# Kernel optimization log

Hardware: AMD Instinct MI355X
Metric: run time of the kernel (lower is better)

The kernel has to match this reference:

```python
import jax, jax.numpy as jnp
import numpy as np

E = 512        # emb_size
H = 2 * E      # LSTM units
B = 512        # beam/query batch (batched Python-loop states)
K = 32         # padded candidates per state
T = 8          # max_path_length
N_ENT = 50000
N_REL = 5000


def setup_inputs() -> dict:
    key = jax.random.key(0)
    ks = jax.random.split(key, 12)
    f32 = jnp.float32
    ent_emb = jax.random.normal(ks[0], (N_ENT, E), f32) * 0.05
    rel_emb = jax.random.normal(ks[1], (N_REL, E), f32) * 0.05
    relation = jax.random.normal(ks[2], (B, E), f32) * 0.05
    Wx = jax.random.normal(ks[3], (H, 4 * H), f32) * 0.02
    Wh = jax.random.normal(ks[4], (H, 4 * H), f32) * 0.02
    b = jnp.zeros((4 * H,), f32)
    W1 = jax.random.normal(ks[5], (4 * E, 3 * E), f32) * 0.02
    b1 = jnp.zeros((3 * E,), f32)
    W2 = jax.random.normal(ks[6], (3 * E, 2 * E), f32) * 0.02
    b2 = jnp.zeros((2 * E,), f32)
    current_ids = jax.random.randint(ks[7], (T, B), 0, N_ENT)
    prev_rel_ids = jax.random.randint(ks[8], (T, B), 0, N_REL)
    cand_rel_ids = jax.random.randint(ks[9], (T, B, K), 0, N_REL)
    cand_ent_ids = jax.random.randint(ks[10], (T, B, K), 0, N_ENT)
    return {
        "ent_emb": ent_emb, "rel_emb": rel_emb, "relation": relation,
        "Wx": Wx, "Wh": Wh, "b": b,
        "W1": W1, "b1": b1, "W2": W2, "b2": b2,
        "current_ids": current_ids, "prev_rel_ids": prev_rel_ids,
        "cand_rel_ids": cand_rel_ids, "cand_ent_ids": cand_ent_ids,
    }


def reference(ent_emb, rel_emb, relation, Wx, Wh, b, W1, b1, W2, b2,
              current_ids, prev_rel_ids, cand_rel_ids, cand_ent_ids):
    Bh = relation.shape[0]
    units = Wh.shape[0]
    h0 = jnp.zeros((Bh, units), ent_emb.dtype)
    c0 = jnp.zeros((Bh, units), ent_emb.dtype)

    def step(carry, xs):
        h, c = carry
        cur, prl, crel, cent = xs
        # LSTMCell input: concat(prev relation vec, current entity vec)  [B, 2E]
        x = jnp.concatenate([rel_emb[prl], ent_emb[cur]], axis=-1)
        z = x @ Wx + h @ Wh + b                      # [B, 4H], keras gate order i,f,g,o
        i_, f_, g_, o_ = jnp.split(z, 4, axis=-1)
        c = jax.nn.sigmoid(f_) * c + jax.nn.sigmoid(i_) * jnp.tanh(g_)
        h = jax.nn.sigmoid(o_) * jnp.tanh(c)
        # posterior MLP on concat(ent, history, relation)  [B, 4E] -> [B, 2E]
        feat = jax.nn.relu(jnp.concatenate([ent_emb[cur], h, relation], axis=-1) @ W1 + b1)
        feat = jax.nn.relu(feat @ W2 + b2)
        # candidate embeddings: concat(rel vec, to-entity vec)  [B, K, 2E]
        cand = jnp.concatenate([rel_emb[crel], ent_emb[cent]], axis=-1)
        probs = jax.nn.softmax(jnp.einsum('bkd,bd->bk', cand, feat), axis=-1)
        return (h, c), probs

    _, probs = jax.lax.scan(step, (h0, c0),
                            (current_ids, prev_rel_ids, cand_rel_ids, cand_ent_ids))
    return probs  # [T, B, K]
```

## Files before the change

kernel.cpp:

```cpp
#include <hip/hip_runtime.h>
#include <stdint.h>

typedef __attribute__((ext_vector_type(4))) float f32x4;
typedef __attribute__((ext_vector_type(8))) __bf16 bf16x8;
typedef __attribute__((ext_vector_type(8))) unsigned short u16x8;
typedef __attribute__((ext_vector_type(4))) unsigned short u16x4;

typedef const __attribute__((address_space(1))) unsigned int gu32;
typedef __attribute__((address_space(3))) unsigned int lu32;

__device__ __forceinline__ float b2f(unsigned short u) {
  unsigned int x = ((unsigned int)u) << 16;
  float f; __builtin_memcpy(&f, &x, 4); return f;
}
__device__ __forceinline__ unsigned short f2b(float f) {
  unsigned int x; __builtin_memcpy(&x, &f, 4);
  x += 0x7fffu + ((x >> 16) & 1u);
  return (unsigned short)(x >> 16);
}
__device__ __forceinline__ float sigmoidf(float x) {
  return 1.f / (1.f + __expf(-x));
}
__device__ __forceinline__ float tanh_fast(float x) {
  return 1.f - 2.f / (1.f + __expf(2.f * x));
}

__global__ __launch_bounds__(256) void prep1(
    const float* __restrict__ Wx, unsigned short* __restrict__ WxT,
    const float* __restrict__ Wh, unsigned short* __restrict__ WhT,
    const float* __restrict__ W1, unsigned short* __restrict__ W1T,
    const float* __restrict__ W2, unsigned short* __restrict__ W2T,
    const float* __restrict__ ent, const float* __restrict__ rel,
    const float* __restrict__ rln,
    const int* __restrict__ cur, const int* __restrict__ prl,
    unsigned short* __restrict__ Xall, unsigned short* __restrict__ ERall) {
  __shared__ unsigned short tile[64][72];
  const int tid = threadIdx.x;
  int b = blockIdx.x;
  if (b < 3200) {
    const float* in; unsigned short* out; int R, C, bx, by;
    if (b < 1024)      { in = Wx; out = WxT; R = 1024; C = 4096; bx = b & 63; by = b >> 6; }
    else if (b < 2048) { b -= 1024; in = Wh; out = WhT; R = 1024; C = 4096; bx = b & 63; by = b >> 6; }
    else if (b < 2816) { b -= 2048; in = W1; out = W1T; R = 2048; C = 1536; bx = b % 24; by = b / 24; }
    else               { b -= 2816; in = W2; out = W2T; R = 1536; C = 1024; bx = b & 15; by = b >> 4; }
    const int r0 = by * 64, c0 = bx * 64;
    const int r = tid >> 3;
    const int c8 = (tid & 7) * 8;
#pragma unroll
    for (int i = 0; i < 2; i++) {
      const int rr = r + 32*i;
      const float* src = in + (size_t)(r0 + rr) * C + c0 + c8;
      f32x4 a = *(const f32x4*)src;
      f32x4 bb = *(const f32x4*)(src + 4);
      unsigned short tmp[8];
#pragma unroll
      for (int j = 0; j < 4; j++) { tmp[j] = f2b(a[j]); tmp[4+j] = f2b(bb[j]); }
      *(u16x8*)(&tile[rr][c8 ^ (((rr >> 3) & 7) << 3)]) = *(u16x8*)tmp;
    }
    __syncthreads();
    const int rswz = (tid & 7) << 3;
#pragma unroll
    for (int i = 0; i < 2; i++) {
      const int ro = r + 32*i;
      unsigned short tmp[8];
#pragma unroll
      for (int j = 0; j < 8; j++) tmp[j] = tile[c8 + j][ro ^ rswz];
      *(u16x8*)(out + (size_t)(c0 + ro) * R + r0 + c8) = *(u16x8*)tmp;
    }
  } else {
    const int row = b - 3200;
    const int bb = row & 511;
    const int ci = cur[row], ri = prl[row];
    const int half = tid >> 7;
    const int j = tid & 127;
    const float* src;
    if (half == 0) src = (j < 64) ? (rel + (size_t)ri * 512 + j * 8)
                                  : (ent + (size_t)ci * 512 + (j - 64) * 8);
    else           src = (j < 64) ? (ent + (size_t)ci * 512 + j * 8)
                                  : (rln + (size_t)bb * 512 + (j - 64) * 8);
    f32x4 a = *(const f32x4*)src, c = *(const f32x4*)(src + 4);
    unsigned short t[8];
#pragma unroll
    for (int q = 0; q < 4; q++) { t[q] = f2b(a[q]); t[4+q] = f2b(c[q]); }
    unsigned short* dst = (half == 0 ? Xall : ERall) + (size_t)row * 1024 + j * 8;
    *(u16x8*)dst = *(u16x8*)t;
  }
}

template<bool HAS_BIAS, bool DO_RELU, bool PERM_B, bool ASPLIT, bool LSTM0, bool FUSE_CONV>
__global__ __launch_bounds__(256) void gemm_bf16(
    const unsigned short* __restrict__ A,
    const unsigned short* __restrict__ A2, int lda,
    const unsigned short* __restrict__ BT, int ldb, int K,
    const float* __restrict__ bias,
    unsigned short* __restrict__ Cout, int ldc,
    const float* __restrict__ gbias,
    unsigned short* __restrict__ Hout, float* __restrict__ Cst,
    const float* __restrict__ entF, unsigned short* __restrict__ entB,
    const float* __restrict__ relF, unsigned short* __restrict__ relB) {
  __shared__ unsigned short As[128][64];
  __shared__ unsigned short Bs[128][64];
  const int tid = threadIdx.x;
  if (FUSE_CONV && blockIdx.y >= 32) {
    const long long N0 = 50000LL * 512 / 8, N1 = 5000LL * 512 / 8;
    long long i = ((long long)(blockIdx.y - 32) * gridDim.x + blockIdx.x) * 256 + tid;
    if (i >= N0 + N1) return;
    const float* in; unsigned short* out;
    if (i < N0) { in = entF; out = entB; }
    else        { in = relF; out = relB; i -= N0; }
    f32x4 a = *(const f32x4*)(in + i * 8);
    f32x4 c = *(const f32x4*)(in + i * 8 + 4);
    unsigned short t[8];
#pragma unroll
    for (int q = 0; q < 4; q++) { t[q] = f2b(a[q]); t[4+q] = f2b(c[q]); }
    *(u16x8*)(out + i * 8) = *(u16x8*)t;
    return;
  }
  const int lane = tid & 63;
  const int w = tid >> 6;
  const int wr = w >> 1, wc = w & 1;
  const int m0 = blockIdx.y * 128, n0 = blockIdx.x * 128;
  f32x4 acc[4][4] = {};
  const int srow = lane >> 3;
  const int scol = ((lane & 7) ^ srow) * 8;

  for (int k0 = 0; k0 < K; k0 += 64) {
    const unsigned short* asrc; int ac;
    if (ASPLIT) {
      if (k0 < 512)       { asrc = A;  ac = k0; }
      else if (k0 < 1536) { asrc = A2; ac = k0 - 512; }
      else                { asrc = A;  ac = k0 - 1024; }
    } else { asrc = A; ac = k0; }
#pragma unroll
    for (int i = 0; i < 4; i++) {
      const int c = w * 4 + i;
      const int row = c * 8 + srow;
      __builtin_amdgcn_global_load_lds(
          (gu32*)(asrc + (size_t)(m0 + row) * lda + ac + scol),
          (lu32*)(&As[0][0] + c * 512), 16, 0, 0);
      const int brow = n0 + row;
      const int prow = PERM_B ? (((brow & 3) << 10) + (brow >> 2)) : brow;
      __builtin_amdgcn_global_load_lds(
          (gu32*)(BT + (size_t)prow * ldb + k0 + scol),
          (lu32*)(&Bs[0][0] + c * 512), 16, 0, 0);
    }
    __syncthreads();
#pragma unroll
    for (int ks = 0; ks < 2; ks++) {
      const int kb = ks * 32 + (lane >> 4) * 8;
      const int kswz = kb ^ ((lane & 7) << 3);
      bf16x8 af[4], bfr[4];
#pragma unroll
      for (int m = 0; m < 4; m++)
        af[m] = *reinterpret_cast<const bf16x8*>(&As[wr*64 + m*16 + (lane & 15)][kswz]);
#pragma unroll
      for (int n = 0; n < 4; n++)
        bfr[n] = *reinterpret_cast<const bf16x8*>(&Bs[wc*64 + n*16 + (lane & 15)][kswz]);
#pragma unroll
      for (int m = 0; m < 4; m++)
#pragma unroll
        for (int n = 0; n < 4; n++)
          acc[m][n] = __builtin_amdgcn_mfma_f32_16x16x32_bf16(af[m], bfr[n], acc[m][n], 0, 0, 0);
    }
    __syncthreads();
  }

  const int cn = lane & 15, rb = (lane >> 4) * 4;
  if (LSTM0 && m0 < 512) {
    const int g = lane & 3;
#pragma unroll
    for (int m = 0; m < 4; m++) {
#pragma unroll
      for (int n = 0; n < 4; n++) {
        const int gn = n0 + wc*64 + n*16 + cn;
        const int u = gn >> 2;
        const float gb = gbias[g * 1024 + u];
        const int row0 = m0 + wr*64 + m*16 + rb;
        const float v0 = acc[m][n][0] + gb;
        const float v1 = acc[m][n][1] + gb;
        const float v2 = acc[m][n][2] + gb;
        const float v3 = acc[m][n][3] + gb;
        auto sel = [&](int idx) {
          return idx == 0 ? v0 : idx == 1 ? v1 : idx == 2 ? v2 : v3;
        };
        const float own = sel(g);
        const float r1 = __shfl_xor(sel(g ^ 1), 1);
        const float r2 = __shfl_xor(sel(g ^ 2), 2);
        const float r3 = __shfl_xor(sel(g ^ 3), 3);
        const float zi = g==0 ? own : g==1 ? r1 : g==2 ? r2 : r3;
        const float zg_= g==0 ? r2  : g==1 ? r3 : g==2 ? own: r1;
        const float zo = g==0 ? r3  : g==1 ? r2 : g==2 ? r1 : own;
        const float cnew = sigmoidf(zi) * tanh_fast(zg_);
        const float h = sigmoidf(zo) * tanh_fast(cnew);
        const size_t hidx = (size_t)(row0 + g) * 1024 + u;
        Cst[hidx] = cnew;
        Hout[hidx] = f2b(h);
      }
    }
    return;
  }
#pragma unroll
  for (int m = 0; m < 4; m++) {
#pragma unroll
    for (int n = 0; n < 4; n++) {
      const int gn = n0 + wc*64 + n*16 + cn;
#pragma unroll
      for (int r = 0; r < 4; r++) {
        const int gm = m0 + wr*64 + m*16 + rb + r;
        float v = acc[m][n][r];
        if (HAS_BIAS) v += bias[gn];
        if (DO_RELU)  v = v > 0.f ? v : 0.f;
        Cout[(size_t)gm * ldc + gn] = f2b(v);
      }
    }
  }
}

__global__ __launch_bounds__(512) void zgemm_lstm(
    const unsigned short* __restrict__ A,
    const unsigned short* __restrict__ BT,
    const unsigned short* __restrict__ pre,
    const float* __restrict__ bias,
    unsigned short* __restrict__ Hout,
    float* __restrict__ Cst) {
  __shared__ unsigned short As[2][2][64][64];
  __shared__ unsigned short Bs[2][2][64][64];
  __shared__ f32x4 accL[4][256];
  const int tid = threadIdx.x;
  const int lane = tid & 63;
  const int w = tid >> 6;
  const int q = w >> 2;
  const int wq = w & 3;
  const int wr = wq >> 1, wc = wq & 1;
  const int m0 = blockIdx.y * 64, n0 = blockIdx.x * 64;
  f32x4 acc[2][2] = {};
  const int tq = tid & 255;
  const int srow = lane >> 3;
  const int scol = ((lane & 7) ^ srow) * 8;

  auto STAGE = [&](int buf, int k0) {
    const int kk = q * 512 + k0;
#pragma unroll
    for (int i = 0; i < 2; i++) {
      const int c = wq * 2 + i;
      const int row = c * 8 + srow;
      __builtin_amdgcn_global_load_lds(
          (gu32*)(A + (size_t)(m0 + row) * 1024 + kk + scol),
          (lu32*)(&As[buf][q][0][0] + c * 512), 16, 0, 0);
      const int brow = n0 + row;
      const int prow = ((brow & 3) << 10) + (brow >> 2);
      __builtin_amdgcn_global_load_lds(
          (gu32*)(BT + (size_t)prow * 1024 + kk + scol),
          (lu32*)(&Bs[buf][q][0][0] + c * 512), 16, 0, 0);
    }
  };

  STAGE(0, 0);
  __syncthreads();
  for (int k0 = 0; k0 < 512; k0 += 64) {
    const int buf = (k0 >> 6) & 1;
    if (k0 + 64 < 512) STAGE(buf ^ 1, k0 + 64);
#pragma unroll
    for (int ks = 0; ks < 2; ks++) {
      const int kb = ks * 32 + (lane >> 4) * 8;
      const int kswz = kb ^ ((lane & 7) << 3);
      bf16x8 af[2], bfr[2];
#pragma unroll
      for (int m = 0; m < 2; m++)
        af[m] = *reinterpret_cast<const bf16x8*>(&As[buf][q][wr*32 + m*16 + (lane & 15)][kswz]);
#pragma unroll
      for (int n = 0; n < 2; n++)
        bfr[n] = *reinterpret_cast<const bf16x8*>(&Bs[buf][q][wc*32 + n*16 + (lane & 15)][kswz]);
#pragma unroll
      for (int m = 0; m < 2; m++)
#pragma unroll
        for (int n = 0; n < 2; n++)
          acc[m][n] = __builtin_amdgcn_mfma_f32_16x16x32_bf16(af[m], bfr[n], acc[m][n], 0, 0, 0);
    }
    __syncthreads();
  }

  if (q == 1) {
#pragma unroll
    for (int m = 0; m < 2; m++)
#pragma unroll
      for (int n = 0; n < 2; n++)
        accL[m*2 + n][tq] = acc[m][n];
  }
  __syncthreads();
  if (q == 0) {
    const int cn = lane & 15, rb = (lane >> 4) * 4, g = lane & 3;
#pragma unroll
    for (int m = 0; m < 2; m++) {
#pragma unroll
      for (int n = 0; n < 2; n++) {
        const f32x4 s4 = accL[m*2 + n][tq];
        const int gn = n0 + wc*32 + n*16 + cn;
        const int u = gn >> 2;
        const float gb = bias[g * 1024 + u];
        const int row0 = m0 + wr*32 + m*16 + rb;
        const float v0 = acc[m][n][0] + s4[0] + b2f(pre[(size_t)(row0+0) * 4096 + gn]) + gb;
        const float v1 = acc[m][n][1] + s4[1] + b2f(pre[(size_t)(row0+1) * 4096 + gn]) + gb;
        const float v2 = acc[m][n][2] + s4[2] + b2f(pre[(size_t)(row0+2) * 4096 + gn]) + gb;
        const float v3 = acc[m][n][3] + s4[3] + b2f(pre[(size_t)(row0+3) * 4096 + gn]) + gb;
        auto sel = [&](int idx) {
          return idx == 0 ? v0 : idx == 1 ? v1 : idx == 2 ? v2 : v3;
        };
        const float own = sel(g);
        const float r1 = __shfl_xor(sel(g ^ 1), 1);
        const float r2 = __shfl_xor(sel(g ^ 2), 2);
        const float r3 = __shfl_xor(sel(g ^ 3), 3);
        const float zi = g==0 ? own : g==1 ? r1 : g==2 ? r2 : r3;
        const float zf = g==0 ? r1  : g==1 ? own: g==2 ? r3 : r2;
        const float zg_= g==0 ? r2  : g==1 ? r3 : g==2 ? own: r1;
        const float zo = g==0 ? r3  : g==1 ? r2 : g==2 ? r1 : own;
        const size_t hidx = (size_t)(row0 + g) * 1024 + u;
        const float cnew = sigmoidf(zf) * Cst[hidx] + sigmoidf(zi) * tanh_fast(zg_);
        const float h = sigmoidf(zo) * tanh_fast(cnew);
        Cst[hidx] = cnew;
        Hout[hidx] = f2b(h);
      }
    }
  }
}

__global__ __launch_bounds__(256) void score_softmax(
    const unsigned short* __restrict__ F2,
    const unsigned short* __restrict__ relB,
    const unsigned short* __restrict__ entB,
    const int* __restrict__ crel, const int* __restrict__ cent,
    float* __restrict__ outp) {
  const int b = blockIdx.x;
  const int tid = threadIdx.x;
  const int lane = tid & 63, w = tid >> 6;
  __shared__ float feat[1024];
  __shared__ float logits[32];
  {
    u16x4 fv = ((const u16x4*)(F2 + (size_t)b * 1024))[tid];
#pragma unroll
    for (int j = 0; j < 4; j++) feat[tid * 4 + j] = b2f(fv[j]);
  }
  __syncthreads();
  for (int k = w; k < 32; k += 4) {
    const int ri = crel[b * 32 + k], ei = cent[b * 32 + k];
    u16x8 rv = *(const u16x8*)(relB + (size_t)ri * 512 + lane * 8);
    u16x8 ev = *(const u16x8*)(entB + (size_t)ei * 512 + lane * 8);
    float sum = 0.f;
#pragma unroll
    for (int j = 0; j < 8; j++) {
      sum += b2f(rv[j]) * feat[lane * 8 + j];
      sum += b2f(ev[j]) * feat[512 + lane * 8 + j];
    }
#pragma unroll
    for (int off = 32; off; off >>= 1) sum += __shfl_down(sum, off, 64);
    if (lane == 0) logits[k] = sum;
  }
  __syncthreads();
  if (tid < 32) {
    const float l = logits[tid];
    float mx = l;
#pragma unroll
    for (int off = 16; off; off >>= 1) mx = fmaxf(mx, __shfl_xor(mx, off, 32));
    const float p = __expf(l - mx);
    float s = p;
#pragma unroll
    for (int off = 16; off; off >>= 1) s += __shfl_xor(s, off, 32);
    outp[(size_t)b * 32 + tid] = p / s;
  }
}

extern "C" void kernel_launch(void* const* d_in, const int* in_sizes, int n_in,
                              void* d_out, int out_size, void* d_ws, size_t ws_size,
                              hipStream_t stream) {
  const float* ent      = (const float*)d_in[0];
  const float* rel      = (const float*)d_in[1];
  const float* relation = (const float*)d_in[2];
  const float* Wx       = (const float*)d_in[3];
  const float* Wh       = (const float*)d_in[4];
  const float* bvec     = (const float*)d_in[5];
  const float* W1       = (const float*)d_in[6];
  const float* b1       = (const float*)d_in[7];
  const float* W2       = (const float*)d_in[8];
  const float* b2       = (const float*)d_in[9];
  const int* cur  = (const int*)d_in[10];
  const int* prl  = (const int*)d_in[11];
  const int* crel = (const int*)d_in[12];
  const int* cent = (const int*)d_in[13];
  float* out = (float*)d_out;
  (void)in_sizes; (void)n_in; (void)out_size; (void)ws_size;

  char* wsp = (char*)d_ws;
  auto alloc = [&](size_t bytes) { char* p = wsp; wsp += (bytes + 255) & ~(size_t)255; return p; };
  unsigned short* entB = (unsigned short*)alloc((size_t)50000 * 512 * 2);
  unsigned short* relB = (unsigned short*)alloc((size_t)5000 * 512 * 2);
  unsigned short* WxT  = (unsigned short*)alloc((size_t)4096 * 1024 * 2);
  unsigned short* WhT  = (unsigned short*)alloc((size_t)4096 * 1024 * 2);
  unsigned short* W1T  = (unsigned short*)alloc((size_t)1536 * 2048 * 2);
  unsigned short* W2T  = (unsigned short*)alloc((size_t)1024 * 1536 * 2);
  unsigned short* Xall = (unsigned short*)alloc((size_t)4096 * 1024 * 2);
  unsigned short* ERall= (unsigned short*)alloc((size_t)4096 * 1024 * 2);
  unsigned short* P1   = (unsigned short*)alloc((size_t)4096 * 4096 * 2);
  unsigned short* Hall = (unsigned short*)alloc((size_t)4096 * 1024 * 2);
  unsigned short* F1   = (unsigned short*)alloc((size_t)4096 * 1536 * 2);
  unsigned short* F2   = (unsigned short*)alloc((size_t)4096 * 1024 * 2);
  float*          C    = (float*)         alloc((size_t)512 * 1024 * 4);

  const dim3 blk(256);
  const size_t HS = (size_t)512 * 1024;

  prep1<<<7296, blk, 0, stream>>>(
      Wx, WxT, Wh, WhT, W1, W1T, W2, W2T,
      ent, rel, relation, cur, prl, Xall, ERall);

  gemm_bf16<false,false,true,false,true,true><<<dim3(32, 32 + 430), blk, 0, stream>>>(
      Xall, nullptr, 1024, WxT, 1024, 1024, nullptr, P1, 4096, bvec, Hall, C,
      ent, entB, rel, relB);

  for (int t = 1; t < 8; t++) {
    zgemm_lstm<<<dim3(64, 8), dim3(512), 0, stream>>>(
        Hall + (size_t)(t - 1) * HS, WhT,
        P1 + (size_t)t * 512 * 4096, bvec,
        Hall + (size_t)t * HS, C);
  }

  gemm_bf16<true,true,false,true,false,false><<<dim3(12, 32), blk, 0, stream>>>(
      ERall, Hall, 1024, W1T, 2048, 2048, b1, F1, 1536, nullptr, nullptr, nullptr,
      nullptr, nullptr, nullptr, nullptr);
  gemm_bf16<true,true,false,false,false,false><<<dim3(8, 32), blk, 0, stream>>>(
      F1, nullptr, 1536, W2T, 1536, 1536, b2, F2, 1024, nullptr, nullptr, nullptr,
      nullptr, nullptr, nullptr, nullptr);

  score_softmax<<<4096, 256, 0, stream>>>(F2, relB, entB, crel, cent, out);
}
```

Baseline: 292.7 us.

## Drop split-K in LSTM step kernel and grid-stride the fused embedding conversion

The recurrent LSTM GEMM kernel no longer splits K across two 256-thread halves that were reduced through LDS. It now uses 256-thread blocks that each loop over the full K=1024, which removes the LDS reduction and the extra barrier but doubles the serial K-loop per block. The fused fp32-to-bf16 embedding conversion in the first GEMM now uses a grid-stride loop over 64 extra block rows instead of 430. Fewer conversion blocks are meant to compete with the GEMM blocks, at the cost of more work per conversion thread.

```diff
diff --git a/kernel.cpp b/kernel.cpp
--- a/kernel.cpp
+++ b/kernel.cpp
@@ -102,18 +102,20 @@
   __shared__ unsigned short Bs[128][64];
   const int tid = threadIdx.x;
   if (FUSE_CONV && blockIdx.y >= 32) {
-    const long long N0 = 50000LL * 512 / 8, N1 = 5000LL * 512 / 8;
+    const long long N0 = 50000LL * 512 / 8, NT = N0 + 5000LL * 512 / 8;
+    const long long nthr = (long long)(gridDim.y - 32) * gridDim.x * 256;
     long long i = ((long long)(blockIdx.y - 32) * gridDim.x + blockIdx.x) * 256 + tid;
-    if (i >= N0 + N1) return;
-    const float* in; unsigned short* out;
-    if (i < N0) { in = entF; out = entB; }
-    else        { in = relF; out = relB; i -= N0; }
-    f32x4 a = *(const f32x4*)(in + i * 8);
-    f32x4 c = *(const f32x4*)(in + i * 8 + 4);
-    unsigned short t[8];
-#pragma unroll
-    for (int q = 0; q < 4; q++) { t[q] = f2b(a[q]); t[4+q] = f2b(c[q]); }
-    *(u16x8*)(out + i * 8) = *(u16x8*)t;
+    for (; i < NT; i += nthr) {
+      const float* in; unsigned short* out; long long j = i;
+      if (j < N0) { in = entF; out = entB; }
+      else        { in = relF; out = relB; j -= N0; }
+      f32x4 a = *(const f32x4*)(in + j * 8);
+      f32x4 c = *(const f32x4*)(in + j * 8 + 4);
+      unsigned short t[8];
+#pragma unroll
+      for (int q = 0; q < 4; q++) { t[q] = f2b(a[q]); t[4+q] = f2b(c[q]); }
+      *(u16x8*)(out + j * 8) = *(u16x8*)t;
+    }
     return;
   }
   const int lane = tid & 63;
@@ -216,50 +218,45 @@
   }
 }
 
-__global__ __launch_bounds__(512) void zgemm_lstm(
+__global__ __launch_bounds__(256) void zgemm_lstm(
     const unsigned short* __restrict__ A,
     const unsigned short* __restrict__ BT,
     const unsigned short* __restrict__ pre,
     const float* __restrict__ bias,
     unsigned short* __restrict__ Hout,
     float* __restrict__ Cst) {
-  __shared__ unsigned short As[2][2][64][64];
-  __shared__ unsigned short Bs[2][2][64][64];
-  __shared__ f32x4 accL[4][256];
+  __shared__ unsigned short As[2][64][64];
+  __shared__ unsigned short Bs[2][64][64];
   const int tid = threadIdx.x;
   const int lane = tid & 63;
   const int w = tid >> 6;
-  const int q = w >> 2;
-  const int wq = w & 3;
-  const int wr = wq >> 1, wc = wq & 1;
+  const int wr = w >> 1, wc = w & 1;
   const int m0 = blockIdx.y * 64, n0 = blockIdx.x * 64;
   f32x4 acc[2][2] = {};
-  const int tq = tid & 255;
   const int srow = lane >> 3;
   const int scol = ((lane & 7) ^ srow) * 8;
 
   auto STAGE = [&](int buf, int k0) {
-    const int kk = q * 512 + k0;
 #pragma unroll
     for (int i = 0; i < 2; i++) {
-      const int c = wq * 2 + i;
+      const int c = w * 2 + i;
       const int row = c * 8 + srow;
       __builtin_amdgcn_global_load_lds(
-          (gu32*)(A + (size_t)(m0 + row) * 1024 + kk + scol),
-          (lu32*)(&As[buf][q][0][0] + c * 512), 16, 0, 0);
+          (gu32*)(A + (size_t)(m0 + row) * 1024 + k0 + scol),
+          (lu32*)(&As[buf][0][0] + c * 512), 16, 0, 0);
       const int brow = n0 + row;
       const int prow = ((brow & 3) << 10) + (brow >> 2);
       __builtin_amdgcn_global_load_lds(
-          (gu32*)(BT + (size_t)prow * 1024 + kk + scol),
-          (lu32*)(&Bs[buf][q][0][0] + c * 512), 16, 0, 0);
+          (gu32*)(BT + (size_t)prow * 1024 + k0 + scol),
+          (lu32*)(&Bs[buf][0][0] + c * 512), 16, 0, 0);
     }
   };
 
   STAGE(0, 0);
   __syncthreads();
-  for (int k0 = 0; k0 < 512; k0 += 64) {
+  for (int k0 = 0; k0 < 1024; k0 += 64) {
     const int buf = (k0 >> 6) & 1;
-    if (k0 + 64 < 512) STAGE(buf ^ 1, k0 + 64);
+    if (k0 + 64 < 1024) STAGE(buf ^ 1, k0 + 64);
 #pragma unroll
     for (int ks = 0; ks < 2; ks++) {
       const int kb = ks * 32 + (lane >> 4) * 8;
@@ -267,10 +264,10 @@
       bf16x8 af[2], bfr[2];
 #pragma unroll
       for (int m = 0; m < 2; m++)
-        af[m] = *reinterpret_cast<const bf16x8*>(&As[buf][q][wr*32 + m*16 + (lane & 15)][kswz]);
+        af[m] = *reinterpret_cast<const bf16x8*>(&As[buf][wr*32 + m*16 + (lane & 15)][kswz]);
 #pragma unroll
       for (int n = 0; n < 2; n++)
-        bfr[n] = *reinterpret_cast<const bf16x8*>(&Bs[buf][q][wc*32 + n*16 + (lane & 15)][kswz]);
+        bfr[n] = *reinterpret_cast<const bf16x8*>(&Bs[buf][wc*32 + n*16 + (lane & 15)][kswz]);
 #pragma unroll
       for (int m = 0; m < 2; m++)
 #pragma unroll
@@ -280,46 +277,35 @@
     __syncthreads();
   }
 
-  if (q == 1) {
-#pragma unroll
-    for (int m = 0; m < 2; m++)
-#pragma unroll
-      for (int n = 0; n < 2; n++)
-        accL[m*2 + n][tq] = acc[m][n];
-  }
-  __syncthreads();
-  if (q == 0) {
-    const int cn = lane & 15, rb = (lane >> 4) * 4, g = lane & 3;
-#pragma unroll
-    for (int m = 0; m < 2; m++) {
-#pragma unroll
-      for (int n = 0; n < 2; n++) {
-        const f32x4 s4 = accL[m*2 + n][tq];
-        const int gn = n0 + wc*32 + n*16 + cn;
-        const int u = gn >> 2;
-        const float gb = bias[g * 1024 + u];
-        const int row0 = m0 + wr*32 + m*16 + rb;
-        const float v0 = acc[m][n][0] + s4[0] + b2f(pre[(size_t)(row0+0) * 4096 + gn]) + gb;
-        const float v1 = acc[m][n][1] + s4[1] + b2f(pre[(size_t)(row0+1) * 4096 + gn]) + gb;
-        const float v2 = acc[m][n][2] + s4[2] + b2f(pre[(size_t)(row0+2) * 4096 + gn]) + gb;
-        const float v3 = acc[m][n][3] + s4[3] + b2f(pre[(size_t)(row0+3) * 4096 + gn]) + gb;
-        auto sel = [&](int idx) {
-          return idx == 0 ? v0 : idx == 1 ? v1 : idx == 2 ? v2 : v3;
-        };
-        const float own = sel(g);
-        const float r1 = __shfl_xor(sel(g ^ 1), 1);
-        const float r2 = __shfl_xor(sel(g ^ 2), 2);
-        const float r3 = __shfl_xor(sel(g ^ 3), 3);
-        const float zi = g==0 ? own : g==1 ? r1 : g==2 ? r2 : r3;
-        const float zf = g==0 ? r1  : g==1 ? own: g==2 ? r3 : r2;
-        const float zg_= g==0 ? r2  : g==1 ? r3 : g==2 ? own: r1;
-        const float zo = g==0 ? r3  : g==1 ? r2 : g==2 ? r1 : own;
-        const size_t hidx = (size_t)(row0 + g) * 1024 + u;
-        const float cnew = sigmoidf(zf) * Cst[hidx] + sigmoidf(zi) * tanh_fast(zg_);
-        const float h = sigmoidf(zo) * tanh_fast(cnew);
-        Cst[hidx] = cnew;
-        Hout[hidx] = f2b(h);
-      }
+  const int cn = lane & 15, rb = (lane >> 4) * 4, g = lane & 3;
+#pragma unroll
+  for (int m = 0; m < 2; m++) {
+#pragma unroll
+    for (int n = 0; n < 2; n++) {
+      const int gn = n0 + wc*32 + n*16 + cn;
+      const int u = gn >> 2;
+      const float gb = bias[g * 1024 + u];
+      const int row0 = m0 + wr*32 + m*16 + rb;
+      const float v0 = acc[m][n][0] + b2f(pre[(size_t)(row0+0) * 4096 + gn]) + gb;
+      const float v1 = acc[m][n][1] + b2f(pre[(size_t)(row0+1) * 4096 + gn]) + gb;
+      const float v2 = acc[m][n][2] + b2f(pre[(size_t)(row0+2) * 4096 + gn]) + gb;
+      const float v3 = acc[m][n][3] + b2f(pre[(size_t)(row0+3) * 4096 + gn]) + gb;
+      auto sel = [&](int idx) {
+        return idx == 0 ? v0 : idx == 1 ? v1 : idx == 2 ? v2 : v3;
+      };
+      const float own = sel(g);
+      const float r1 = __shfl_xor(sel(g ^ 1), 1);
+      const float r2 = __shfl_xor(sel(g ^ 2), 2);
+      const float r3 = __shfl_xor(sel(g ^ 3), 3);
+      const float zi = g==0 ? own : g==1 ? r1 : g==2 ? r2 : r3;
+      const float zf = g==0 ? r1  : g==1 ? own: g==2 ? r3 : r2;
+      const float zg_= g==0 ? r2  : g==1 ? r3 : g==2 ? own: r1;
+      const float zo = g==0 ? r3  : g==1 ? r2 : g==2 ? r1 : own;
+      const size_t hidx = (size_t)(row0 + g) * 1024 + u;
+      const float cnew = sigmoidf(zf) * Cst[hidx] + sigmoidf(zi) * tanh_fast(zg_);
+      const float h = sigmoidf(zo) * tanh_fast(cnew);
+      Cst[hidx] = cnew;
+      Hout[hidx] = f2b(h);
     }
   }
 }
@@ -412,12 +398,12 @@
       Wx, WxT, Wh, WhT, W1, W1T, W2, W2T,
       ent, rel, relation, cur, prl, Xall, ERall);
 
-  gemm_bf16<false,false,true,false,true,true><<<dim3(32, 32 + 430), blk, 0, stream>>>(
+  gemm_bf16<false,false,true,false,true,true><<<dim3(32, 32 + 64), blk, 0, stream>>>(
       Xall, nullptr, 1024, WxT, 1024, 1024, nullptr, P1, 4096, bvec, Hall, C,
       ent, entB, rel, relB);
 
   for (int t = 1; t < 8; t++) {
-    zgemm_lstm<<<dim3(64, 8), dim3(512), 0, stream>>>(
+    zgemm_lstm<<<dim3(64, 8), blk, 0, stream>>>(
         Hall + (size_t)(t - 1) * HS, WhT,
         P1 + (size_t)t * 512 * 4096, bvec,
         Hall + (size_t)t * HS, C);
```

After: 324.0 us. 10.7% more time.
